# Performance work log

Measured on AMD Instinct MI355X. Metric: run time of the kernel, lower is better.

The kernel has to match this reference:

```python
import jax, jax.numpy as jnp
import numpy as np

H, N, I, K = 1024, 16, 128, 2  # model dim, n_experts, expert inner dim (hardcoded in Expert), top-k
B, S = 4, 4096


def setup_inputs() -> dict:
    key = jax.random.key(0)
    ks = jax.random.split(key, 4)
    x = jax.random.normal(ks[0], (B, S, H), jnp.float32)
    Wr = jax.random.normal(ks[1], (N, H), jnp.float32) / np.sqrt(H)      # router Linear(h,n,bias=False) weight [n,h]
    Wg = jax.random.normal(ks[2], (N, I, H), jnp.float32) / np.sqrt(H)   # per-expert g: Linear(h,i) weight [i,h]
    bg = jnp.zeros((N, I), jnp.float32)
    Wu = jax.random.normal(ks[3], (N, H, I), jnp.float32) / np.sqrt(I)   # per-expert u: Linear(i,h) weight [h,i]
    bu = jnp.zeros((N, H), jnp.float32)
    return {"x": x, "Wr": Wr, "Wg": Wg, "bg": bg, "Wu": Wu, "bu": bu, "k": K}


def reference(x, Wr, Wg, bg, Wu, bu, k):
    b, s, h = x.shape
    n = Wr.shape[0]
    xf = x.reshape(-1, h)                      # [T, h]
    T = xf.shape[0]
    logits = xf @ Wr.T                          # [T, n]
    val, idx = jax.lax.top_k(logits, k)         # [T, k]
    w = jax.nn.softmax(val, axis=-1)            # softmax over selected top-k logits
    # scatter top-k weights into a dense [T, n] gate matrix (zero for unselected experts)
    gates = jnp.zeros((T, n), x.dtype).at[jnp.arange(T)[:, None], idx].set(w)
    # all-expert SwiGLU-free MLP: silu(x @ Wg^T + bg) @ Wu^T + bu, weighted combine by gates
    a = jax.nn.silu(jnp.einsum('th,nih->tni', xf, Wg) + bg)   # [T, n, i]
    out = jnp.einsum('tn,tni,nhi->th', gates, a, Wu) + gates @ bu
    return out.reshape(b, s, h)
```

## Files before the change

kernel.cpp:

```cpp
#include <hip/hip_runtime.h>
#include <hip/hip_fp16.h>

#define T_TOK 16384
#define HDIM  1024
#define NE    16
#define IDIM  128
#define BMq   64
#define NSLOT (T_TOK*2)
#define NSLOT_PAD (NSLOT + NE*BMq)
#define NBLK1 (NSLOT_PAD/BMq)

typedef _Float16 half8 __attribute__((ext_vector_type(8)));
typedef _Float16 half4 __attribute__((ext_vector_type(4)));
typedef float    f32x4 __attribute__((ext_vector_type(4)));

#define WS_TOKE 0
#define WS_TOKW 131072
#define WS_CNT  262144
#define WS_CUR  262208
#define WS_OFF  262272
#define WS_STOK 262400
#define WS_SW   397568
#define WS_ABUF 532736
#define WS_TSLOT 9183488ULL
#define WS_X16   17703168ULL
#define WS_OBUF  51257600ULL
#define WS_FULL_END 120463616ULL

__device__ inline void hilo8(float4 a, float4 b, half8& h, half8& l) {
    float f[8] = {a.x, a.y, a.z, a.w, b.x, b.y, b.z, b.w};
#pragma unroll
    for (int i = 0; i < 8; ++i) {
        _Float16 hi = (_Float16)f[i];
        h[i] = hi;
        l[i] = (_Float16)((f[i] - (float)hi) * 2048.f);
    }
}

template<bool WX>
__global__ __launch_bounds__(256) void router_k(const float* __restrict__ x,
                                                const float* __restrict__ Wr,
                                                int2* __restrict__ tok_e,
                                                float2* __restrict__ tok_w,
                                                _Float16* __restrict__ x16,
                                                int* __restrict__ counts,
                                                int* __restrict__ slot_tok) {
    __shared__ float red[4][16][16];
    __shared__ int hist[NE];
    int tid = threadIdx.x;
    int wv = tid >> 6, lane = tid & 63;
    int tile0 = blockIdx.x * 16;

    int gi = blockIdx.x * 256 + tid;
    if (gi < NSLOT_PAD) slot_tok[gi] = -1;
    if (tid < NE) hist[tid] = 0;

    int row = lane & 15;
    int kq  = (lane >> 4) * 8;
    const float* xrow = x  + (size_t)(tile0 + row) * HDIM;
    const float* wrow = Wr + (size_t)row * HDIM;
    f32x4 accM = {0.f,0.f,0.f,0.f};
    f32x4 accC = {0.f,0.f,0.f,0.f};
#pragma unroll
    for (int s = 0; s < 8; ++s) {
        int k = wv * 256 + s * 32 + kq;
        float4 xa = *reinterpret_cast<const float4*>(xrow + k);
        float4 xb = *reinterpret_cast<const float4*>(xrow + k + 4);
        float4 wa = *reinterpret_cast<const float4*>(wrow + k);
        float4 wb = *reinterpret_cast<const float4*>(wrow + k + 4);
        half8 xh, xl, wh, wl;
        hilo8(xa, xb, xh, xl);
        hilo8(wa, wb, wh, wl);
        if (WX)
            *reinterpret_cast<half8*>(x16 + (size_t)(tile0 + row) * HDIM + k) = xh;
        accM = __builtin_amdgcn_mfma_f32_16x16x32_f16(xh, wh, accM, 0, 0, 0);
        accC = __builtin_amdgcn_mfma_f32_16x16x32_f16(xh, wl, accC, 0, 0, 0);
        accC = __builtin_amdgcn_mfma_f32_16x16x32_f16(xl, wh, accC, 0, 0, 0);
    }
#pragma unroll
    for (int j = 0; j < 4; ++j)
        red[wv][(lane >> 4) * 4 + j][lane & 15] = accM[j] + accC[j] * (1.f/2048.f);
    __syncthreads();
    if (tid < 16) {
        float v1 = -1e30f, v2 = -1e30f; int i1 = 0, i2 = 0;
#pragma unroll
        for (int q = 0; q < NE; ++q) {
            float lv = red[0][tid][q] + red[1][tid][q] + red[2][tid][q] + red[3][tid][q];
            if (lv > v1)      { v2 = v1; i2 = i1; v1 = lv; i1 = q; }
            else if (lv > v2) { v2 = lv; i2 = q; }
        }
        int t = tile0 + tid;
        float e2 = __expf(v2 - v1);
        float inv = 1.f / (1.f + e2);
        tok_e[t] = make_int2(i1, i2);
        tok_w[t] = make_float2(inv, e2 * inv);
        atomicAdd(&hist[i1], 1);
        atomicAdd(&hist[i2], 1);
    }
    __syncthreads();
    if (tid < NE) { int c = hist[tid]; if (c) atomicAdd(&counts[tid], c); }
}

__global__ void scan_k(const int* __restrict__ counts, int* __restrict__ offs) {
    if (threadIdx.x == 0) {
        int acc = 0;
        for (int e = 0; e < NE; ++e) {
            offs[e] = acc;
            acc += ((counts[e] + BMq - 1) / BMq) * BMq;
        }
        offs[NE] = acc;
    }
}

template<bool FULL>
__global__ __launch_bounds__(256) void scatter_k(const int2* __restrict__ tok_e,
                                                 const float2* __restrict__ tok_w,
                                                 const int* __restrict__ offs,
                                                 int* __restrict__ cursors,
                                                 int* __restrict__ slot_tok,
                                                 float* __restrict__ slot_w,
                                                 int2* __restrict__ tok_slots) {
    __shared__ int lcnt[NE];
    __shared__ int lbase[NE];
    if (threadIdx.x < NE) lcnt[threadIdx.x] = 0;
    __syncthreads();
    int t = blockIdx.x * 256 + threadIdx.x;
    int2 te = tok_e[t]; float2 tw = tok_w[t];
    int p0 = atomicAdd(&lcnt[te.x], 1);
    int p1 = atomicAdd(&lcnt[te.y], 1);
    __syncthreads();
    if (threadIdx.x < NE)
        lbase[threadIdx.x] = atomicAdd(&cursors[threadIdx.x], lcnt[threadIdx.x]);
    __syncthreads();
    int s0 = offs[te.x] + lbase[te.x] + p0;
    int s1 = offs[te.y] + lbase[te.y] + p1;
    slot_tok[s0] = t; slot_w[s0] = tw.x;
    slot_tok[s1] = t; slot_w[s1] = tw.y;
    if (FULL) tok_slots[t] = make_int2(s0, s1);
}

template<bool FULL>
__global__ __launch_bounds__(256) void gemm1_k(const float* __restrict__ x,
                                               const _Float16* __restrict__ x16,
                                               const float* __restrict__ Wg,
                                               const float* __restrict__ bg,
                                               const int* __restrict__ offs,
                                               const int* __restrict__ slot_tok,
                                               _Float16* __restrict__ abuf) {
    __shared__ __align__(16) _Float16 As[64 * 64];
    __shared__ __align__(16) _Float16 Bs[128 * 64];
    __shared__ int tokLds[64];
    int row0 = blockIdx.x * BMq;
    if (row0 >= offs[NE]) return;
    int e = 0;
#pragma unroll
    for (int q = 1; q < NE; ++q) if (offs[q] <= row0) e = q;
    int tid = threadIdx.x;
    if (tid < 64) tokLds[tid] = slot_tok[row0 + tid];
    __syncthreads();
    int wv = tid >> 6, lane = tid & 63;
    f32x4 acc[4][2] = {};
    for (int kk = 0; kk < HDIM; kk += 64) {
        if (FULL) {
#pragma unroll
            for (int j = 0; j < 2; ++j) {
                int idx = tid + j * 256;
                int r = idx >> 3, hq = idx & 7;
                int tok = tokLds[r];
                half8 v = {0,0,0,0,0,0,0,0};
                if (tok >= 0) v = *reinterpret_cast<const half8*>(x16 + (size_t)tok * HDIM + kk + hq * 8);
                *reinterpret_cast<half8*>(&As[r * 64 + ((hq * 8) ^ ((r & 7) << 3))]) = v;
            }
        } else {
#pragma unroll
            for (int j = 0; j < 4; ++j) {
                int idx = tid + j * 256;
                int r = idx >> 4, kq = idx & 15;
                int tok = tokLds[r];
                float4 v = make_float4(0.f, 0.f, 0.f, 0.f);
                if (tok >= 0) v = *reinterpret_cast<const float4*>(x + (size_t)tok * HDIM + kk + kq * 4);
                half4 hv = {(_Float16)v.x, (_Float16)v.y, (_Float16)v.z, (_Float16)v.w};
                *reinterpret_cast<half4*>(&As[r * 64 + ((kq * 4) ^ ((r & 7) << 3))]) = hv;
            }
        }
#pragma unroll 4
        for (int j = 0; j < 8; ++j) {
            int idx = tid + j * 256;
            int r = idx >> 4, kq = idx & 15;
            float4 v = *reinterpret_cast<const float4*>(Wg + (size_t)e * IDIM * HDIM + (size_t)r * HDIM + kk + kq * 4);
            half4 hv = {(_Float16)v.x, (_Float16)v.y, (_Float16)v.z, (_Float16)v.w};
            *reinterpret_cast<half4*>(&Bs[r * 64 + ((kq * 4) ^ ((r & 7) << 3))]) = hv;
        }
        __syncthreads();
#pragma unroll
        for (int ks = 0; ks < 64; ks += 32) {
            int c = ks + ((lane >> 4) << 3);
            half8 af[4], bf[2];
#pragma unroll
            for (int rt = 0; rt < 4; ++rt) {
                int r = rt * 16 + (lane & 15);
                af[rt] = *reinterpret_cast<const half8*>(&As[r * 64 + (c ^ ((r & 7) << 3))]);
            }
#pragma unroll
            for (int ct = 0; ct < 2; ++ct) {
                int r = wv * 32 + ct * 16 + (lane & 15);
                bf[ct] = *reinterpret_cast<const half8*>(&Bs[r * 64 + (c ^ ((r & 7) << 3))]);
            }
#pragma unroll
            for (int rt = 0; rt < 4; ++rt)
#pragma unroll
                for (int ct = 0; ct < 2; ++ct)
                    acc[rt][ct] = __builtin_amdgcn_mfma_f32_16x16x32_f16(af[rt], bf[ct], acc[rt][ct], 0, 0, 0);
        }
        __syncthreads();
    }
#pragma unroll
    for (int rt = 0; rt < 4; ++rt)
#pragma unroll
        for (int ct = 0; ct < 2; ++ct) {
            int i = wv * 32 + ct * 16 + (lane & 15);
            float bgv = bg[e * IDIM + i];
#pragma unroll
            for (int j = 0; j < 4; ++j) {
                int m = rt * 16 + ((lane >> 4) << 2) + j;
                if (tokLds[m] >= 0) {
                    float v = acc[rt][ct][j] + bgv;
                    float sv = v / (1.f + __expf(-v));
                    abuf[(size_t)(row0 + m) * IDIM + i] = (_Float16)sv;
                }
            }
        }
}

template<bool FULL>
__global__ __launch_bounds__(256) void gemm2_k(const _Float16* __restrict__ abuf,
                                               const float* __restrict__ Wu,
                                               const float* __restrict__ bu,
                                               const int* __restrict__ offs,
                                               const int* __restrict__ slot_tok,
                                               const float* __restrict__ slot_w,
                                               float* __restrict__ out,
                                               _Float16* __restrict__ Obuf) {
    __shared__ __align__(16) _Float16 As[64 * 128];
    __shared__ __align__(16) _Float16 Bs[128 * 128];
    __shared__ int   tokLds[64];
    __shared__ float wLds[64];
    int row0 = blockIdx.x * BMq;
    if (row0 >= offs[NE]) return;
    int h0 = blockIdx.y * 128;
    int e = 0;
#pragma unroll
    for (int q = 1; q < NE; ++q) if (offs[q] <= row0) e = q;
    int tid = threadIdx.x;
    if (tid < 64) { tokLds[tid] = slot_tok[row0 + tid]; wLds[tid] = slot_w[row0 + tid]; }
#pragma unroll
    for (int j = 0; j < 4; ++j) {
        int idx = tid + j * 256;
        int r = idx >> 4, hq = idx & 15;
        half8 v = *reinterpret_cast<const half8*>(abuf + (size_t)(row0 + r) * IDIM + hq * 8);
        *reinterpret_cast<half8*>(&As[r * 128 + ((hq * 8) ^ ((r & 7) << 3))]) = v;
    }
#pragma unroll 4
    for (int j = 0; j < 16; ++j) {
        int idx = tid + j * 256;
        int r = idx >> 5, fq = idx & 31;
        float4 v = *reinterpret_cast<const float4*>(Wu + (size_t)e * HDIM * IDIM + (size_t)(h0 + r) * IDIM + fq * 4);
        half4 hv = {(_Float16)v.x, (_Float16)v.y, (_Float16)v.z, (_Float16)v.w};
        *reinterpret_cast<half4*>(&Bs[r * 128 + ((fq * 4) ^ ((r & 7) << 3))]) = hv;
    }
    __syncthreads();
    int wv = tid >> 6, lane = tid & 63;
    f32x4 acc[4][2] = {};
#pragma unroll
    for (int ks = 0; ks < 128; ks += 32) {
        int c = ks + ((lane >> 4) << 3);
        half8 af[4], bf[2];
#pragma unroll
        for (int rt = 0; rt < 4; ++rt) {
            int r = rt * 16 + (lane & 15);
            af[rt] = *reinterpret_cast<const half8*>(&As[r * 128 + (c ^ ((r & 7) << 3))]);
        }
#pragma unroll
        for (int ct = 0; ct < 2; ++ct) {
            int r = wv * 32 + ct * 16 + (lane & 15);
            bf[ct] = *reinterpret_cast<const half8*>(&Bs[r * 128 + (c ^ ((r & 7) << 3))]);
        }
#pragma unroll
        for (int rt = 0; rt < 4; ++rt)
#pragma unroll
            for (int ct = 0; ct < 2; ++ct)
                acc[rt][ct] = __builtin_amdgcn_mfma_f32_16x16x32_f16(af[rt], bf[ct], acc[rt][ct], 0, 0, 0);
    }
#pragma unroll
    for (int rt = 0; rt < 4; ++rt)
#pragma unroll
        for (int ct = 0; ct < 2; ++ct) {
            int h = h0 + wv * 32 + ct * 16 + (lane & 15);
            float buv = bu[e * HDIM + h];
#pragma unroll
            for (int j = 0; j < 4; ++j) {
                int m = rt * 16 + ((lane >> 4) << 2) + j;
                if (FULL) {
                    Obuf[(size_t)(row0 + m) * HDIM + h] = (_Float16)(acc[rt][ct][j] + buv);
                } else {
                    int tok = tokLds[m];
                    if (tok >= 0)
                        atomicAdd(out + (size_t)tok * HDIM + h,
                                  (acc[rt][ct][j] + buv) * wLds[m]);
                }
            }
        }
}

__global__ __launch_bounds__(256) void combine_k(const _Float16* __restrict__ Obuf,
                                                 const int2* __restrict__ tok_slots,
                                                 const float2* __restrict__ tok_w,
                                                 float* __restrict__ out) {
    int wv = threadIdx.x >> 6, lane = threadIdx.x & 63;
    int t = blockIdx.x * 4 + wv;
    int2   sl = tok_slots[t];
    float2 tw = tok_w[t];
    const _Float16* O1 = Obuf + (size_t)sl.x * HDIM;
    const _Float16* O2 = Obuf + (size_t)sl.y * HDIM;
    float* op = out + (size_t)t * HDIM;
#pragma unroll
    for (int q = 0; q < 4; ++q) {
        int h = q * 256 + lane * 4;
        half4  a1 = *reinterpret_cast<const half4*>(O1 + h);
        half4  a2 = *reinterpret_cast<const half4*>(O2 + h);
        float4 o;
        o.x = tw.x * (float)a1[0] + tw.y * (float)a2[0];
        o.y = tw.x * (float)a1[1] + tw.y * (float)a2[1];
        o.z = tw.x * (float)a1[2] + tw.y * (float)a2[2];
        o.w = tw.x * (float)a1[3] + tw.y * (float)a2[3];
        *reinterpret_cast<float4*>(op + h) = o;
    }
}

extern "C" void kernel_launch(void* const* d_in, const int* in_sizes, int n_in,
                              void* d_out, int out_size, void* d_ws, size_t ws_size,
                              hipStream_t stream) {
    const float* x  = (const float*)d_in[0];
    const float* Wr = (const float*)d_in[1];
    const float* Wg = (const float*)d_in[2];
    const float* bg = (const float*)d_in[3];
    const float* Wu = (const float*)d_in[4];
    const float* bu = (const float*)d_in[5];
    float* out = (float*)d_out;
    char* ws = (char*)d_ws;

    int2*      tok_e    = (int2*)(ws + WS_TOKE);
    float2*    tok_w    = (float2*)(ws + WS_TOKW);
    int*       counts   = (int*)(ws + WS_CNT);
    int*       cursors  = (int*)(ws + WS_CUR);
    int*       offs     = (int*)(ws + WS_OFF);
    int*       slot_tok = (int*)(ws + WS_STOK);
    float*     slot_w   = (float*)(ws + WS_SW);
    _Float16*  abuf     = (_Float16*)(ws + WS_ABUF);
    int2*      tok_slots= (int2*)(ws + WS_TSLOT);
    _Float16*  x16      = (_Float16*)(ws + WS_X16);
    _Float16*  Obuf     = (_Float16*)(ws + WS_OBUF);

    const bool full = (ws_size >= WS_FULL_END);

    hipMemsetAsync(ws + WS_CNT, 0, 256, stream);

    if (full) {
        router_k<true><<<T_TOK/16, 256, 0, stream>>>(x, Wr, tok_e, tok_w, x16, counts, slot_tok);
        scan_k   <<<1, 64, 0, stream>>>(counts, offs);
        scatter_k<true><<<T_TOK/256, 256, 0, stream>>>(tok_e, tok_w, offs, cursors, slot_tok, slot_w, tok_slots);
        gemm1_k<true><<<NBLK1, 256, 0, stream>>>(x, x16, Wg, bg, offs, slot_tok, abuf);
        dim3 g2(NBLK1, 8);
        gemm2_k<true><<<g2, 256, 0, stream>>>(abuf, Wu, bu, offs, slot_tok, slot_w, out, Obuf);
        combine_k<<<T_TOK/4, 256, 0, stream>>>(Obuf, tok_slots, tok_w, out);
    } else {
        hipMemsetAsync(d_out, 0, (size_t)T_TOK * HDIM * sizeof(float), stream);
        router_k<false><<<T_TOK/16, 256, 0, stream>>>(x, Wr, tok_e, tok_w, nullptr, counts, slot_tok);
        scan_k   <<<1, 64, 0, stream>>>(counts, offs);
        scatter_k<false><<<T_TOK/256, 256, 0, stream>>>(tok_e, tok_w, offs, cursors, slot_tok, slot_w, nullptr);
        gemm1_k<false><<<NBLK1, 256, 0, stream>>>(x, nullptr, Wg, bg, offs, slot_tok, abuf);
        dim3 g2(NBLK1, 8);
        gemm2_k<false><<<g2, 256, 0, stream>>>(abuf, Wu, bu, offs, slot_tok, slot_w, out, nullptr);
    }
}
```

Baseline: 274.4 us.

## Pre-convert expert weights to fp16, drop scan kernel, widen gemm1 K-tile

Adds a kernel that converts Wg and Wu to fp16 once per call, so the GEMM kernels load half8 weights instead of converting fp32 on every tile. The separate single-thread scan kernel is removed; expert offsets are now recomputed from counts inside scatter and both GEMMs. gemm1 now uses a 128-wide K step, which doubles its shared memory and halves the number of barriers. The trade-offs are an extra launch and weight pass per call, redundant offset computation in every block, and higher LDS use that may lower occupancy.

```diff
diff --git a/kernel.cpp b/kernel.cpp
--- a/kernel.cpp
+++ b/kernel.cpp
@@ -23,6 +23,8 @@
 #define WS_SW   397568
 #define WS_ABUF 532736
 #define WS_TSLOT 9183488ULL
+#define WS_WG16  9314560ULL
+#define WS_WU16  13508864ULL
 #define WS_X16   17703168ULL
 #define WS_OBUF  51257600ULL
 #define WS_FULL_END 120463616ULL
@@ -35,6 +37,18 @@
         h[i] = hi;
         l[i] = (_Float16)((f[i] - (float)hi) * 2048.f);
     }
+}
+
+__device__ inline void expert_of(const int* __restrict__ counts, int row0,
+                                 int& e, int& total) {
+    int acc = 0; e = 0;
+#pragma unroll
+    for (int q = 0; q < NE; ++q) {
+        int nx = acc + ((counts[q] + BMq - 1) / BMq) * BMq;
+        if (nx <= row0) e = q + 1;
+        acc = nx;
+    }
+    total = acc;
 }
 
 template<bool WX>
@@ -101,28 +115,39 @@
     if (tid < NE) { int c = hist[tid]; if (c) atomicAdd(&counts[tid], c); }
 }
 
-__global__ void scan_k(const int* __restrict__ counts, int* __restrict__ offs) {
-    if (threadIdx.x == 0) {
-        int acc = 0;
-        for (int e = 0; e < NE; ++e) {
-            offs[e] = acc;
-            acc += ((counts[e] + BMq - 1) / BMq) * BMq;
-        }
-        offs[NE] = acc;
-    }
+__global__ __launch_bounds__(256) void cvtw_k(const float* __restrict__ Wg,
+                                              const float* __restrict__ Wu,
+                                              _Float16* __restrict__ Wg16,
+                                              _Float16* __restrict__ Wu16) {
+    int i = blockIdx.x * 256 + threadIdx.x;
+    float4 g = reinterpret_cast<const float4*>(Wg)[i];
+    float4 u = reinterpret_cast<const float4*>(Wu)[i];
+    half4 gh = {(_Float16)g.x,(_Float16)g.y,(_Float16)g.z,(_Float16)g.w};
+    half4 uh = {(_Float16)u.x,(_Float16)u.y,(_Float16)u.z,(_Float16)u.w};
+    reinterpret_cast<half4*>(Wg16)[i] = gh;
+    reinterpret_cast<half4*>(Wu16)[i] = uh;
 }
 
 template<bool FULL>
 __global__ __launch_bounds__(256) void scatter_k(const int2* __restrict__ tok_e,
                                                  const float2* __restrict__ tok_w,
-                                                 const int* __restrict__ offs,
+                                                 const int* __restrict__ counts,
                                                  int* __restrict__ cursors,
                                                  int* __restrict__ slot_tok,
                                                  float* __restrict__ slot_w,
                                                  int2* __restrict__ tok_slots) {
     __shared__ int lcnt[NE];
     __shared__ int lbase[NE];
+    __shared__ int offsLds[NE];
     if (threadIdx.x < NE) lcnt[threadIdx.x] = 0;
+    if (threadIdx.x == 0) {
+        int acc = 0;
+#pragma unroll
+        for (int e = 0; e < NE; ++e) {
+            offsLds[e] = acc;
+            acc += ((counts[e] + BMq - 1) / BMq) * BMq;
+        }
+    }
     __syncthreads();
     int t = blockIdx.x * 256 + threadIdx.x;
     int2 te = tok_e[t]; float2 tw = tok_w[t];
@@ -132,8 +157,8 @@
     if (threadIdx.x < NE)
         lbase[threadIdx.x] = atomicAdd(&cursors[threadIdx.x], lcnt[threadIdx.x]);
     __syncthreads();
-    int s0 = offs[te.x] + lbase[te.x] + p0;
-    int s1 = offs[te.y] + lbase[te.y] + p1;
+    int s0 = offsLds[te.x] + lbase[te.x] + p0;
+    int s1 = offsLds[te.y] + lbase[te.y] + p1;
     slot_tok[s0] = t; slot_w[s0] = tw.x;
     slot_tok[s1] = t; slot_w[s1] = tw.y;
     if (FULL) tok_slots[t] = make_int2(s0, s1);
@@ -143,68 +168,75 @@
 __global__ __launch_bounds__(256) void gemm1_k(const float* __restrict__ x,
                                                const _Float16* __restrict__ x16,
                                                const float* __restrict__ Wg,
+                                               const _Float16* __restrict__ Wg16,
                                                const float* __restrict__ bg,
-                                               const int* __restrict__ offs,
+                                               const int* __restrict__ counts,
                                                const int* __restrict__ slot_tok,
                                                _Float16* __restrict__ abuf) {
-    __shared__ __align__(16) _Float16 As[64 * 64];
-    __shared__ __align__(16) _Float16 Bs[128 * 64];
+    __shared__ __align__(16) _Float16 As[64 * 128];
+    __shared__ __align__(16) _Float16 Bs[128 * 128];
     __shared__ int tokLds[64];
     int row0 = blockIdx.x * BMq;
-    if (row0 >= offs[NE]) return;
-    int e = 0;
-#pragma unroll
-    for (int q = 1; q < NE; ++q) if (offs[q] <= row0) e = q;
+    int e, total;
+    expert_of(counts, row0, e, total);
+    if (row0 >= total) return;
     int tid = threadIdx.x;
     if (tid < 64) tokLds[tid] = slot_tok[row0 + tid];
     __syncthreads();
     int wv = tid >> 6, lane = tid & 63;
     f32x4 acc[4][2] = {};
-    for (int kk = 0; kk < HDIM; kk += 64) {
+    for (int kk = 0; kk < HDIM; kk += 128) {
         if (FULL) {
 #pragma unroll
-            for (int j = 0; j < 2; ++j) {
+            for (int j = 0; j < 4; ++j) {
                 int idx = tid + j * 256;
-                int r = idx >> 3, hq = idx & 7;
+                int r = idx >> 4, hq = idx & 15;
                 int tok = tokLds[r];
                 half8 v = {0,0,0,0,0,0,0,0};
                 if (tok >= 0) v = *reinterpret_cast<const half8*>(x16 + (size_t)tok * HDIM + kk + hq * 8);
-                *reinterpret_cast<half8*>(&As[r * 64 + ((hq * 8) ^ ((r & 7) << 3))]) = v;
+                *reinterpret_cast<half8*>(&As[r * 128 + ((hq * 8) ^ ((r & 7) << 3))]) = v;
+            }
+#pragma unroll 4
+            for (int j = 0; j < 8; ++j) {
+                int idx = tid + j * 256;
+                int r = idx >> 4, hq = idx & 15;
+                half8 v = *reinterpret_cast<const half8*>(Wg16 + (size_t)e * IDIM * HDIM + (size_t)r * HDIM + kk + hq * 8);
+                *reinterpret_cast<half8*>(&Bs[r * 128 + ((hq * 8) ^ ((r & 7) << 3))]) = v;
             }
         } else {
 #pragma unroll
-            for (int j = 0; j < 4; ++j) {
+            for (int j = 0; j < 8; ++j) {
                 int idx = tid + j * 256;
-                int r = idx >> 4, kq = idx & 15;
+                int r = idx >> 5, kq = idx & 31;
                 int tok = tokLds[r];
                 float4 v = make_float4(0.f, 0.f, 0.f, 0.f);
                 if (tok >= 0) v = *reinterpret_cast<const float4*>(x + (size_t)tok * HDIM + kk + kq * 4);
                 half4 hv = {(_Float16)v.x, (_Float16)v.y, (_Float16)v.z, (_Float16)v.w};
-                *reinterpret_cast<half4*>(&As[r * 64 + ((kq * 4) ^ ((r & 7) << 3))]) = hv;
-            }
-        }
+                *reinterpret_cast<half4*>(&As[r * 128 + ((kq * 4) ^ ((r & 7) << 3))]) = hv;
+            }
 #pragma unroll 4
-        for (int j = 0; j < 8; ++j) {
-            int idx = tid + j * 256;
-            int r = idx >> 4, kq = idx & 15;
-            float4 v = *reinterpret_cast<const float4*>(Wg + (size_t)e * IDIM * HDIM + (size_t)r * HDIM + kk + kq * 4);
-            half4 hv = {(_Float16)v.x, (_Float16)v.y, (_Float16)v.z, (_Float16)v.w};
-            *reinterpret_cast<half4*>(&Bs[r * 64 + ((kq * 4) ^ ((r & 7) << 3))]) = hv;
+            for (int j = 0; j < 16; ++j) {
+                int idx = tid + j * 256;
+                int r = idx >> 5, kq = idx & 31;
+                float4 v = *reinterpret_cast<const float4*>(Wg + (size_t)e * IDIM * HDIM + (size_t)r * HDIM + kk + kq * 4);
+                half4 hv = {(_Float16)v.x, (_Float16)v.y, (_Float16)v.z, (_Float16)v.w};
+                *reinterpret_cast<half4*>(&Bs[r * 128 + ((kq * 4) ^ ((r & 7) << 3))]) = hv;
+            }
         }
         __syncthreads();
 #pragma unroll
-        for (int ks = 0; ks < 64; ks += 32) {
+        for (int ks = 0; ks < 128; ks += 32) {
             int c = ks + ((lane >> 4) << 3);
             half8 af[4], bf[2];
 #pragma unroll
             for (int rt = 0; rt < 4; ++rt) {
                 int r = rt * 16 + (lane & 15);
-                af[rt] = *reinterpret_cast<const half8*>(&As[r * 64 + (c ^ ((r & 7) << 3))]);
+                af[rt] = *reinterpret_cast<const half8*>(&As[r * 128 + (c ^ ((r & 7) << 3))]);
             }
 #pragma unroll
             for (int ct = 0; ct < 2; ++ct) {
                 int r = wv * 32 + ct * 16 + (lane & 15);
-                bf[ct] = *reinterpret_cast<const half8*>(&Bs[r * 64 + (c ^ ((r & 7) << 3))]);
+                bf[ct] = *reinterpret_cast<const half8*>(&Bs[r * 128 + (c ^ ((r & 7) << 3))]);
             }
 #pragma unroll
             for (int rt = 0; rt < 4; ++rt)
@@ -235,8 +267,9 @@
 template<bool FULL>
 __global__ __launch_bounds__(256) void gemm2_k(const _Float16* __restrict__ abuf,
                                                const float* __restrict__ Wu,
+                                               const _Float16* __restrict__ Wu16,
                                                const float* __restrict__ bu,
-                                               const int* __restrict__ offs,
+                                               const int* __restrict__ counts,
                                                const int* __restrict__ slot_tok,
                                                const float* __restrict__ slot_w,
                                                float* __restrict__ out,
@@ -246,11 +279,10 @@
     __shared__ int   tokLds[64];
     __shared__ float wLds[64];
     int row0 = blockIdx.x * BMq;
-    if (row0 >= offs[NE]) return;
+    int e, total;
+    expert_of(counts, row0, e, total);
+    if (row0 >= total) return;
     int h0 = blockIdx.y * 128;
-    int e = 0;
-#pragma unroll
-    for (int q = 1; q < NE; ++q) if (offs[q] <= row0) e = q;
     int tid = threadIdx.x;
     if (tid < 64) { tokLds[tid] = slot_tok[row0 + tid]; wLds[tid] = slot_w[row0 + tid]; }
 #pragma unroll
@@ -260,13 +292,23 @@
         half8 v = *reinterpret_cast<const half8*>(abuf + (size_t)(row0 + r) * IDIM + hq * 8);
         *reinterpret_cast<half8*>(&As[r * 128 + ((hq * 8) ^ ((r & 7) << 3))]) = v;
     }
+    if (FULL) {
 #pragma unroll 4
-    for (int j = 0; j < 16; ++j) {
-        int idx = tid + j * 256;
-        int r = idx >> 5, fq = idx & 31;
-        float4 v = *reinterpret_cast<const float4*>(Wu + (size_t)e * HDIM * IDIM + (size_t)(h0 + r) * IDIM + fq * 4);
-        half4 hv = {(_Float16)v.x, (_Float16)v.y, (_Float16)v.z, (_Float16)v.w};
-        *reinterpret_cast<half4*>(&Bs[r * 128 + ((fq * 4) ^ ((r & 7) << 3))]) = hv;
+        for (int j = 0; j < 8; ++j) {
+            int idx = tid + j * 256;
+            int r = idx >> 4, fq = idx & 15;
+            half8 v = *reinterpret_cast<const half8*>(Wu16 + (size_t)e * HDIM * IDIM + (size_t)(h0 + r) * IDIM + fq * 8);
+            *reinterpret_cast<half8*>(&Bs[r * 128 + ((fq * 8) ^ ((r & 7) << 3))]) = v;
+        }
+    } else {
+#pragma unroll 4
+        for (int j = 0; j < 16; ++j) {
+            int idx = tid + j * 256;
+            int r = idx >> 5, fq = idx & 31;
+            float4 v = *reinterpret_cast<const float4*>(Wu + (size_t)e * HDIM * IDIM + (size_t)(h0 + r) * IDIM + fq * 4);
+            half4 hv = {(_Float16)v.x, (_Float16)v.y, (_Float16)v.z, (_Float16)v.w};
+            *reinterpret_cast<half4*>(&Bs[r * 128 + ((fq * 4) ^ ((r & 7) << 3))]) = hv;
+        }
     }
     __syncthreads();
     int wv = tid >> 6, lane = tid & 63;
@@ -353,11 +395,12 @@
     float2*    tok_w    = (float2*)(ws + WS_TOKW);
     int*       counts   = (int*)(ws + WS_CNT);
     int*       cursors  = (int*)(ws + WS_CUR);
-    int*       offs     = (int*)(ws + WS_OFF);
     int*       slot_tok = (int*)(ws + WS_STOK);
     float*     slot_w   = (float*)(ws + WS_SW);
     _Float16*  abuf     = (_Float16*)(ws + WS_ABUF);
     int2*      tok_slots= (int2*)(ws + WS_TSLOT);
+    _Float16*  Wg16     = (_Float16*)(ws + WS_WG16);
+    _Float16*  Wu16     = (_Float16*)(ws + WS_WU16);
     _Float16*  x16      = (_Float16*)(ws + WS_X16);
     _Float16*  Obuf     = (_Float16*)(ws + WS_OBUF);
 
@@ -366,20 +409,19 @@
     hipMemsetAsync(ws + WS_CNT, 0, 256, stream);
 
     if (full) {
+        cvtw_k   <<<2048, 256, 0, stream>>>(Wg, Wu, Wg16, Wu16);
         router_k<true><<<T_TOK/16, 256, 0, stream>>>(x, Wr, tok_e, tok_w, x16, counts, slot_tok);
-        scan_k   <<<1, 64, 0, stream>>>(counts, offs);
-        scatter_k<true><<<T_TOK/256, 256, 0, stream>>>(tok_e, tok_w, offs, cursors, slot_tok, slot_w, tok_slots);
-        gemm1_k<true><<<NBLK1, 256, 0, stream>>>(x, x16, Wg, bg, offs, slot_tok, abuf);
+        scatter_k<true><<<T_TOK/256, 256, 0, stream>>>(tok_e, tok_w, counts, cursors, slot_tok, slot_w, tok_slots);
+        gemm1_k<true><<<NBLK1, 256, 0, stream>>>(x, x16, Wg, Wg16, bg, counts, slot_tok, abuf);
         dim3 g2(NBLK1, 8);
-        gemm2_k<true><<<g2, 256, 0, stream>>>(abuf, Wu, bu, offs, slot_tok, slot_w, out, Obuf);
+        gemm2_k<true><<<g2, 256, 0, stream>>>(abuf, Wu, Wu16, bu, counts, slot_tok, slot_w, out, Obuf);
         combine_k<<<T_TOK/4, 256, 0, stream>>>(Obuf, tok_slots, tok_w, out);
     } else {
         hipMemsetAsync(d_out, 0, (size_t)T_TOK * HDIM * sizeof(float), stream);
         router_k<false><<<T_TOK/16, 256, 0, stream>>>(x, Wr, tok_e, tok_w, nullptr, counts, slot_tok);
-        scan_k   <<<1, 64, 0, stream>>>(counts, offs);
-        scatter_k<false><<<T_TOK/256, 256, 0, stream>>>(tok_e, tok_w, offs, cursors, slot_tok, slot_w, nullptr);
-        gemm1_k<false><<<NBLK1, 256, 0, stream>>>(x, nullptr, Wg, bg, offs, slot_tok, abuf);
+        scatter_k<false><<<T_TOK/256, 256, 0, stream>>>(tok_e, tok_w, counts, cursors, slot_tok, slot_w, nullptr);
+        gemm1_k<false><<<NBLK1, 256, 0, stream>>>(x, nullptr, Wg, nullptr, bg, counts, slot_tok, abuf);
         dim3 g2(NBLK1, 8);
-        gemm2_k<false><<<g2, 256, 0, stream>>>(abuf, Wu, bu, offs, slot_tok, slot_w, out, nullptr);
-    }
-}
+        gemm2_k<false><<<g2, 256, 0, stream>>>(abuf, Wu, nullptr, bu, counts, slot_tok, slot_w, out, nullptr);
+    }
+}
```

Result: faster. 245.6 us (-10.5%).
